# Performance work log

Hardware: AMD Instinct MI355X
Metric: run time of the kernel (lower is better)

Reference implementation:

```python
import jax, jax.numpy as jnp
import numpy as np

HIDDEN = 1024
FRAME = 171
B = 128
T = 256


def _uniform(key, shape, fan):
    bound = 1.0 / np.sqrt(fan)
    return jax.random.uniform(key, shape, jnp.float32, -bound, bound)


def setup_inputs() -> dict:
    key = jax.random.key(0)
    ks = jax.random.split(key, 16)
    H, C = HIDDEN, FRAME
    inp = {
        "seq": jax.random.normal(ks[0], (B, T, C), jnp.float32),
        # LSTMCell 1 (input C -> H); torch layout: weight_ih [4H, in], weight_hh [4H, H]
        "w_ih1": _uniform(ks[1], (4 * H, C), H),
        "w_hh1": _uniform(ks[2], (4 * H, H), H),
        "b_ih1": _uniform(ks[3], (4 * H,), H),
        "b_hh1": _uniform(ks[4], (4 * H,), H),
        # LSTMCell 2 (H -> H)
        "w_ih2": _uniform(ks[5], (4 * H, H), H),
        "w_hh2": _uniform(ks[6], (4 * H, H), H),
        "b_ih2": _uniform(ks[7], (4 * H,), H),
        "b_hh2": _uniform(ks[8], (4 * H,), H),
        # LSTMCell 3 (H -> H)
        "w_ih3": _uniform(ks[9], (4 * H, H), H),
        "w_hh3": _uniform(ks[10], (4 * H, H), H),
        "b_ih3": _uniform(ks[11], (4 * H,), H),
        "b_hh3": _uniform(ks[12], (4 * H,), H),
        # Linear decoder H -> C
        "dec_w": _uniform(ks[13], (C, H), H),
        "dec_b": _uniform(ks[14], (C,), H),
        "gt": 5,
        "cond": 5,
    }
    return inp


def _lstm_cell(x, h, c, w_ih, w_hh, b_ih, b_hh):
    # torch.nn.LSTMCell: gates ordered (i, f, g, o)
    z = x @ w_ih.T + h @ w_hh.T + (b_ih + b_hh)  # [B, 4H]
    i, f, g, o = jnp.split(z, 4, axis=-1)
    c_new = jax.nn.sigmoid(f) * c + jax.nn.sigmoid(i) * jnp.tanh(g)
    h_new = jax.nn.sigmoid(o) * jnp.tanh(c_new)
    return h_new, c_new


def reference(seq, w_ih1, w_hh1, b_ih1, b_hh1,
              w_ih2, w_hh2, b_ih2, b_hh2,
              w_ih3, w_hh3, b_ih3, b_hh3,
              dec_w, dec_b, gt, cond):
    b, t, c = seq.shape
    h = seq.dtype
    # auto-conditioning pattern: gt ground-truth frames then cond self-fed frames
    pattern = (jnp.arange(t) % (gt + cond)) < gt  # [T] bool
    H = w_hh1.shape[1]
    zeros_h = jnp.zeros((b, H), h)
    init = (zeros_h, zeros_h, zeros_h, zeros_h, zeros_h, zeros_h,
            jnp.zeros((b, c), h))

    def step(carry, xs):
        h1, c1, h2, c2, h3, c3, xo = carry
        x_t, p_t = xs
        inp = jnp.where(p_t, x_t, xo)
        h1, c1 = _lstm_cell(inp, h1, c1, w_ih1, w_hh1, b_ih1, b_hh1)
        h2, c2 = _lstm_cell(h1, h2, c2, w_ih2, w_hh2, b_ih2, b_hh2)
        h3, c3 = _lstm_cell(h2, h3, c3, w_ih3, w_hh3, b_ih3, b_hh3)
        out = h3 @ dec_w.T + dec_b  # [B, C]
        return (h1, c1, h2, c2, h3, c3, out), out

    seq_t = jnp.transpose(seq, (1, 0, 2))  # [T, B, C]
    _, outs = jax.lax.scan(step, init, (seq_t, pattern))
    return jnp.transpose(outs, (1, 0, 2))  # [B, T, C]
```

## Files before the change

kernel.cpp:

```cpp
#include <hip/hip_runtime.h>
#include <math.h>

#define TSTEPS 256
#define CDIM 171
#define XSTR 6400
#define SEQB (TSTEPS*CDIM)

#define ARR_OFF   0
#define GF_OFF    2048
#define REL_OFF   2560
#define XCNT_OFF  3072
#define GREG_OFF  3080
#define ARR2_OFF  4096
#define NFLAGS    8192

typedef short v8s __attribute__((ext_vector_type(8)));
typedef float v4f __attribute__((ext_vector_type(4)));
typedef unsigned int v4u __attribute__((ext_vector_type(4)));

static __device__ __forceinline__ unsigned short f2bf(float f) {
  unsigned int u = __float_as_uint(f);
  u += 0x7fffu + ((u >> 16) & 1u);
  return (unsigned short)(u >> 16);
}
static __device__ __forceinline__ float bf2f(unsigned short h) {
  return __uint_as_float(((unsigned int)h) << 16);
}
static __device__ __forceinline__ float sigf(float x) { return 1.0f / (1.0f + expf(-x)); }

static __device__ __forceinline__ bool probe_bf16(const unsigned int* w) {
  int c = 0;
  #pragma unroll
  for (int i = 0; i < 8; ++i) {
    unsigned e = (w[i] >> 7) & 0xFFu;
    c += (e >= 90u && e <= 145u) ? 1 : 0;
  }
  return c == 8;
}
static __device__ __forceinline__ float getv(const void* p, bool bf, size_t i) {
  return bf ? bf2f(((const unsigned short*)p)[i]) : ((const float*)p)[i];
}

static __device__ __forceinline__ unsigned ld_agent(const unsigned* p) {
  return __hip_atomic_load(p, __ATOMIC_RELAXED, __HIP_MEMORY_SCOPE_AGENT);
}
static __device__ __forceinline__ void st_agent(unsigned* p, unsigned v) {
  __hip_atomic_store(p, v, __ATOMIC_RELAXED, __HIP_MEMORY_SCOPE_AGENT);
}
static __device__ __forceinline__ void st_short_sys(unsigned short* p, unsigned short v) {
  asm volatile("global_store_short %0, %1, off sc0 sc1"
               :: "v"(p), "v"((unsigned)v) : "memory");
}
static __device__ __forceinline__ v4u ld_b128_sys(const unsigned short* p) {
  v4u v;
  asm volatile("global_load_dwordx4 %0, %1, off sc0 sc1\n\ts_waitcnt vmcnt(0)"
               : "=v"(v) : "v"(p) : "memory");
  return v;
}

__global__ __launch_bounds__(256) void init_kernel(
    const void* seq, const void* wih1, const void* whh1,
    const void* bih1, const void* bhh1,
    const void* wih2, const void* whh2, const void* bih2, const void* bhh2,
    const void* wih3, const void* whh3, const void* bih3, const void* bhh3,
    const void* decw,
    unsigned short* __restrict__ X, float* __restrict__ BS,
    unsigned* __restrict__ flags,
    unsigned short* __restrict__ WL1, unsigned short* __restrict__ WL2,
    unsigned short* __restrict__ WL3, unsigned short* __restrict__ WDEC,
    unsigned short* __restrict__ XR, unsigned short* __restrict__ XGT,
    const int* __restrict__ gtp, const int* __restrict__ condp)
{
  const int tid = blockIdx.x * 256 + threadIdx.x;
  const int NT = 2048 * 256;
  const bool bfm = probe_bf16((const unsigned int*)seq);
  int gt = gtp[0];
  const bool p0 = 0 < gt;

  for (int i = tid; i < 128 * XSTR; i += NT) {
    int b = i / XSTR, c = i - b * XSTR;
    unsigned short v = 0;
    if (c < CDIM && p0) v = f2bf(getv(seq, bfm, (size_t)b * SEQB + c));
    X[i] = v;
  }
  for (int i = tid; i < 8 * 128 * XSTR; i += NT) {
    int r = i % (128 * XSTR);
    int b = r / XSTR, c = r - b * XSTR;
    unsigned short v = 0;
    if (c < CDIM && p0) v = f2bf(getv(seq, bfm, (size_t)b * SEQB + c));
    XR[i] = v;
  }
  const void* bis[3] = {bih1, bih2, bih3};
  const void* bhs[3] = {bhh1, bhh2, bhh3};
  for (int i = tid; i < 3 * 4096; i += NT) {
    int l = i >> 12, n = i & 4095;
    BS[i] = getv(bis[l], bfm, n) + getv(bhs[l], bfm, n);
  }
  for (int i = tid; i < NFLAGS; i += NT) flags[i] = 0u;
  for (int i = tid; i < 4096 * 1280; i += NT) {
    int r = i / 1280, c = i - r * 1280;
    float v;
    if (c < CDIM)      v = getv(wih1, bfm, (size_t)r * CDIM + c);
    else if (c < 256)  v = 0.f;
    else               v = getv(whh1, bfm, (size_t)r * 1024 + (c - 256));
    WL1[i] = f2bf(v);
  }
  for (int i = tid; i < 4096 * 2048; i += NT) {
    int r = i >> 11, c = i & 2047;
    size_t o = (size_t)r * 1024 + (c & 1023);
    WL2[i] = f2bf((c < 1024) ? getv(wih2, bfm, o) : getv(whh2, bfm, o));
    WL3[i] = f2bf((c < 1024) ? getv(wih3, bfm, o) : getv(whh3, bfm, o));
  }
  for (int i = tid; i < 176 * 1024; i += NT) {
    int r = i >> 10, c = i & 1023;
    WDEC[i] = (r < CDIM) ? f2bf(getv(decw, bfm, (size_t)r * 1024 + c)) : (unsigned short)0;
  }
  if (XGT) {
    for (int i = tid; i < TSTEPS * 128 * 256; i += NT) {
      int t = i >> 15, b = (i >> 8) & 127, c = i & 255;
      unsigned short v = 0;
      if (c < CDIM) v = f2bf(getv(seq, bfm, (size_t)b * SEQB + (size_t)t * CDIM + c));
      XGT[i] = v;
    }
  }
}

static __device__ __forceinline__ void gbar_nf(
    unsigned* fl, unsigned xcd, unsigned rank, unsigned NX, unsigned amask,
    unsigned G, int wave, int lane, unsigned& budget)
{
  __syncthreads();
  if (threadIdx.x == 0) st_agent(fl + ARR_OFF + xcd * 256 + rank, G);
  if (wave == 0) {
    if (rank == 0) {
      const unsigned* ab = fl + ARR_OFF + xcd * 256;
      for (;;) {
        unsigned ok = 1u;
        #pragma unroll
        for (int k = 0; k < 4; ++k) {
          unsigned r = (unsigned)lane + 64u * k;
          if (r < NX) ok &= (ld_agent(ab + r) >= G) ? 1u : 0u;
        }
        if (__all((int)ok)) break;
        if (budget == 0) break;
        --budget; __builtin_amdgcn_s_sleep(1);
      }
      st_agent(fl + GF_OFF + xcd * 64, G);
      for (;;) {
        unsigned ok = 1u;
        if (lane < 8 && ((amask >> lane) & 1u))
          ok = (ld_agent(fl + GF_OFF + (unsigned)lane * 64) >= G) ? 1u : 0u;
        if (__all((int)ok)) break;
        if (budget == 0) break;
        --budget; __builtin_amdgcn_s_sleep(1);
      }
      st_agent(fl + REL_OFF + xcd * 64, G);
    } else {
      unsigned* rp = fl + REL_OFF + xcd * 64;
      for (;;) {
        unsigned v = ld_agent(rp);
        if (__all((int)(v >= G))) break;
        if (budget == 0) break;
        --budget; __builtin_amdgcn_s_sleep(1);
      }
    }
  }
  __syncthreads();
}

static __device__ __forceinline__ void xcopy(
    unsigned short* __restrict__ dst, const unsigned short* __restrict__ src,
    int hoff, int nchunks, int rowshift, unsigned rank, unsigned NX, int tid)
{
  const int mask = (1 << rowshift) - 1;
  for (unsigned c = rank * 256u + (unsigned)tid; c < (unsigned)nchunks;
       c += NX * 256u) {
    int row = (int)(c >> rowshift);
    size_t off = (size_t)row * XSTR + hoff + ((size_t)(c & mask) << 3);
    v4u v = ld_b128_sys(src + off);
    *(v4u*)(dst + off) = v;
  }
}

static __device__ __forceinline__ void xbar(
    unsigned* fl, unsigned xcd, unsigned rank, unsigned NX,
    unsigned G, int wave, int lane, unsigned& budget)
{
  __syncthreads();
  if (threadIdx.x == 0) st_agent(fl + ARR2_OFF + xcd * 256 + rank, G);
  if (wave == 0) {
    const unsigned* ab = fl + ARR2_OFF + xcd * 256;
    for (;;) {
      unsigned ok = 1u;
      #pragma unroll
      for (int k = 0; k < 4; ++k) {
        unsigned r = (unsigned)lane + 64u * k;
        if (r < NX) ok &= (ld_agent(ab + r) >= G) ? 1u : 0u;
      }
      if (__all((int)ok)) break;
      if (budget == 0) break;
      --budget; __builtin_amdgcn_s_sleep(1);
    }
    asm volatile("buffer_inv" ::: "memory");
  }
  __syncthreads();
}

template<int NCH>
static __device__ __forceinline__ void mfma_phase(
    const v8s* wf, const unsigned short* __restrict__ Xb,
    int a0, int bnd, int a1, int kbase, v4f* acc)
{
  #pragma unroll
  for (int i = 0; i < 8; ++i) acc[i] = (v4f){0.f, 0.f, 0.f, 0.f};
  #pragma unroll
  for (int c = 0; c < NCH; ++c) {
    const int acol = kbase + 32 * c;
    const int xcol = (acol < bnd) ? (a0 + acol) : (a1 + acol - bnd);
    const unsigned short* ap = Xb + xcol;
    #pragma unroll
    for (int m = 0; m < 8; ++m) {
      v8s a = *(const v8s*)(ap + (size_t)(16 * m) * XSTR);
      acc[m] = __builtin_amdgcn_mfma_f32_16x16x32_bf16(a, wf[c], acc[m], 0, 0, 0);
    }
  }
}

static __device__ __forceinline__ void lstm_epilogue(
    v4f* acc, float* lred, int wave, int lane,
    const float* bs4, float* cst2,
    unsigned short* __restrict__ X, int hoff, int g)
{
  const int l15 = lane & 15, quad = lane >> 4;
  float* myp = lred + wave * 2048;
  #pragma unroll
  for (int m = 0; m < 8; ++m)
    #pragma unroll
    for (int j = 0; j < 4; ++j)
      myp[m * 256 + l15 * 16 + ((4 * quad + j) ^ ((l15 >> 1) & 3))] = acc[m][j];
  __syncthreads();
  const int ri = lane >> 2, hc = lane & 3;
  #pragma unroll
  for (int e = 0; e < 2; ++e) {
    const int m = 2 * wave + e;
    float z[4];
    #pragma unroll
    for (int k = 0; k < 4; ++k) z[k] = bs4[k];
    #pragma unroll
    for (int w2 = 0; w2 < 4; ++w2) {
      const float* pp = lred + w2 * 2048 + m * 256;
      #pragma unroll
      for (int k = 0; k < 4; ++k) {
        const int col = hc + 4 * k;
        z[k] += pp[col * 16 + (ri ^ ((col >> 1) & 3))];
      }
    }
    float cn = sigf(z[1]) * cst2[e] + sigf(z[0]) * tanhf(z[2]);
    float h  = sigf(z[3]) * tanhf(cn);
    cst2[e] = cn;
    const int row = 32 * wave + 16 * e + ri;
    st_short_sys(X + (size_t)row * XSTR + hoff + 4 * g + hc, f2bf(h));
  }
}

__global__ __launch_bounds__(256, 1) void persist(
    const unsigned short* __restrict__ WL1, const unsigned short* __restrict__ WL2,
    const unsigned short* __restrict__ WL3, const unsigned short* __restrict__ WDEC,
    const float* __restrict__ BS, unsigned short* __restrict__ X,
    unsigned* __restrict__ flags, unsigned short* __restrict__ XR,
    const void* __restrict__ seq, const void* __restrict__ decb,
    void* __restrict__ outp, const unsigned short* __restrict__ XGT,
    const int* __restrict__ gtp, const int* __restrict__ condp)
{
  const int g = blockIdx.x;
  const int tid = threadIdx.x, wave = tid >> 6, lane = tid & 63;
  const int l15 = lane & 15, quad = lane >> 4;
  const bool bf = probe_bf16((const unsigned int*)seq);
  int gt = gtp[0]; int per = gt + condp[0]; if (per < 1) per = 1;
  unsigned budget = 20000000u;

  __shared__ unsigned s_rank;
  unsigned xcd;
  asm volatile("s_getreg_b32 %0, hwreg(HW_REG_XCC_ID)" : "=s"(xcd));
  xcd &= 7u;
  if (tid == 0) {
    s_rank = __hip_atomic_fetch_add(flags + XCNT_OFF + xcd, 1u,
                                    __ATOMIC_RELAXED, __HIP_MEMORY_SCOPE_AGENT);
    __hip_atomic_fetch_add(flags + GREG_OFF, 1u,
                           __ATOMIC_RELEASE, __HIP_MEMORY_SCOPE_AGENT);
  }
  __syncthreads();
  const unsigned rank = s_rank;
  if (wave == 0 && lane == 0) {
    while (__hip_atomic_load(flags + GREG_OFF, __ATOMIC_ACQUIRE,
                             __HIP_MEMORY_SCOPE_AGENT) < 256u) {
      if (budget == 0) break;
      --budget; __builtin_amdgcn_s_sleep(4);
    }
  }
  __syncthreads();
  const unsigned NX = ld_agent(flags + XCNT_OFF + xcd);
  unsigned amask = 0;
  #pragma unroll
  for (int k = 0; k < 8; ++k)
    amask |= (ld_agent(flags + XCNT_OFF + k) > 0u ? 1u : 0u) << k;

  unsigned short* XRb = XR + (size_t)xcd * (128 * XSTR);

  const int br = 1024 * (l15 >> 2) + 4 * g + (l15 & 3);
  v8s w1f[10], w2f[16], w3f[16], wdf[8];
  {
    const unsigned short* p = WL1 + (size_t)br * 1280 + 320 * wave + 8 * quad;
    #pragma unroll
    for (int c = 0; c < 10; ++c) w1f[c] = *(const v8s*)(p + 32 * c);
  }
  {
    const unsigned short* p = WL2 + (size_t)br * 2048 + 512 * wave + 8 * quad;
    #pragma unroll
    for (int c = 0; c < 16; ++c) w2f[c] = *(const v8s*)(p + 32 * c);
  }
  {
    const unsigned short* p = WL3 + (size_t)br * 2048 + 512 * wave + 8 * quad;
    #pragma unroll
    for (int c = 0; c < 16; ++c) w3f[c] = *(const v8s*)(p + 32 * c);
  }
  const int dm = g / 11, dn = g - dm * 11;
  if (g < 88) {
    const unsigned short* p = WDEC + (size_t)(16 * dn + l15) * 1024 + 256 * wave + 8 * quad;
    #pragma unroll
    for (int c = 0; c < 8; ++c) wdf[c] = *(const v8s*)(p + 32 * c);
  } else {
    #pragma unroll
    for (int c = 0; c < 8; ++c) wdf[c] = (v8s){0, 0, 0, 0, 0, 0, 0, 0};
  }
  float bsr[3][4];
  #pragma unroll
  for (int l = 0; l < 3; ++l)
    #pragma unroll
    for (int gm = 0; gm < 4; ++gm)
      bsr[l][gm] = BS[4096 * l + 1024 * gm + 4 * g + (lane & 3)];
  float dbv = 0.f;
  if (g < 88) { int col = 16 * dn + l15; if (col < CDIM) dbv = getv(decb, bf, col); }

  float cst1[2] = {0.f, 0.f}, cst2v[2] = {0.f, 0.f}, cst3[2] = {0.f, 0.f};
  __shared__ float lred[8192];
  const unsigned short* Xb = XRb + (size_t)l15 * XSTR + 8 * quad;
  unsigned bgen = 0;
  v4f acc[8];

  for (int t = 0; t < TSTEPS; ++t) {
    const int p_ = t & 1, q_ = p_ ^ 1;
    const bool pt = (t % per) < gt;
    if (t > 0 && !pt) {
      gbar_nf(flags, xcd, rank, NX, amask, ++bgen, wave, lane, budget);
      xcopy(XRb, X, 0, 4096, 5, rank, NX, tid);
      xbar(flags, xcd, rank, NX, bgen, wave, lane, budget);
    }

    if (pt && wave == 0) {
      #pragma unroll
      for (int i = 0; i < 8; ++i) acc[i] = (v4f){0.f, 0.f, 0.f, 0.f};
      if (XGT) {
        const unsigned short* xb = XGT + ((size_t)t * 128 + l15) * 256 + 8 * quad;
        #pragma unroll
        for (int c = 0; c < 8; ++c) {
          #pragma unroll
          for (int m = 0; m < 8; ++m) {
            v8s a = *(const v8s*)(xb + 32 * c + (size_t)(16 * m) * 256);
            acc[m] = __builtin_amdgcn_mfma_f32_16x16x32_bf16(a, w1f[c], acc[m], 0, 0, 0);
          }
        }
      } else {
        #pragma unroll
        for (int c = 0; c < 8; ++c) {
          const int col0 = 32 * c + 8 * quad;
          #pragma unroll
          for (int m = 0; m < 8; ++m) {
            const size_t so = (size_t)(l15 + 16 * m) * SEQB + (size_t)t * CDIM;
            v8s a;
            #pragma unroll
            for (int j = 0; j < 8; ++j) {
              const int cc = col0 + j;
              unsigned short hv = 0;
              if (cc < CDIM)
                hv = bf ? ((const unsigned short*)seq)[so + cc]
                        : f2bf(((const float*)seq)[so + cc]);
              a[j] = (short)hv;
            }
            acc[m] = __builtin_amdgcn_mfma_f32_16x16x32_bf16(a, w1f[c], acc[m], 0, 0, 0);
          }
        }
      }
      #pragma unroll
      for (int c = 8; c < 10; ++c) {
        const unsigned short* ap = Xb + (256 + 1024 * q_) + (32 * c - 256);
        #pragma unroll
        for (int m = 0; m < 8; ++m) {
          v8s a = *(const v8s*)(ap + (size_t)(16 * m) * XSTR);
          acc[m] = __builtin_amdgcn_mfma_f32_16x16x32_bf16(a, w1f[c], acc[m], 0, 0, 0);
        }
      }
    } else {
      mfma_phase<10>(w1f, Xb, 0, 256, 256 + 1024 * q_, 320 * wave, acc);
    }
    lstm_epilogue(acc, lred, wave, lane, bsr[0], cst1, X, 256 + 1024 * p_, g);

    gbar_nf(flags, xcd, rank, NX, amask, ++bgen, wave, lane, budget);
    xcopy(XRb, X, 256 + 1024 * p_, 16384, 7, rank, NX, tid);
    xbar(flags, xcd, rank, NX, bgen, wave, lane, budget);
    mfma_phase<16>(w2f, Xb, 256 + 1024 * p_, 1024, 2304 + 1024 * q_, 512 * wave, acc);
    lstm_epilogue(acc, lred, wave, lane, bsr[1], cst2v, X, 2304 + 1024 * p_, g);

    gbar_nf(flags, xcd, rank, NX, amask, ++bgen, wave, lane, budget);
    xcopy(XRb, X, 2304 + 1024 * p_, 16384, 7, rank, NX, tid);
    xbar(flags, xcd, rank, NX, bgen, wave, lane, budget);
    mfma_phase<16>(w3f, Xb, 2304 + 1024 * p_, 1024, 4352 + 1024 * q_, 512 * wave, acc);
    lstm_epilogue(acc, lred, wave, lane, bsr[2], cst3, X, 4352 + 1024 * p_, g);

    gbar_nf(flags, xcd, rank, NX, amask, ++bgen, wave, lane, budget);
    xcopy(XRb, X, 4352 + 1024 * p_, 16384, 7, rank, NX, tid);
    xbar(flags, xcd, rank, NX, bgen, wave, lane, budget);
    if (g < 88) {
      v4f da = (v4f){0.f, 0.f, 0.f, 0.f};
      const unsigned short* ap = XRb + (size_t)(16 * dm + l15) * XSTR
                               + (4352 + 1024 * p_) + 256 * wave + 8 * quad;
      #pragma unroll
      for (int c = 0; c < 8; ++c) {
        v8s a = *(const v8s*)(ap + 32 * c);
        da = __builtin_amdgcn_mfma_f32_16x16x32_bf16(a, wdf[c], da, 0, 0, 0);
      }
      float* myp = lred + wave * 2048;
      #pragma unroll
      for (int j = 0; j < 4; ++j)
        myp[l15 * 16 + ((4 * quad + j) ^ ((l15 >> 1) & 3))] = da[j];
      __syncthreads();
      if (wave == 0) {
        const int col = 16 * dn + l15;
        const bool pnext = ((t + 1) % per) < gt;
        #pragma unroll
        for (int e = 0; e < 4; ++e) {
          const int r = 4 * e + quad;
          float v = dbv;
          #pragma unroll
          for (int w2 = 0; w2 < 4; ++w2)
            v += lred[w2 * 2048 + l15 * 16 + (r ^ ((l15 >> 1) & 3))];
          if (col < CDIM) {
            const int brow = 16 * dm + r;
            const size_t oidx = (size_t)brow * SEQB + (size_t)t * CDIM + col;
            if (bf) ((unsigned short*)outp)[oidx] = f2bf(v);
            else    ((float*)outp)[oidx] = v;
            if (t < TSTEPS - 1 && !pnext)
              st_short_sys(X + (size_t)brow * XSTR + col, f2bf(v));
          }
        }
      }
      __syncthreads();
    }
  }
}

extern "C" void kernel_launch(void* const* d_in, const int* in_sizes, int n_in,
                              void* d_out, int out_size, void* d_ws, size_t ws_size,
                              hipStream_t stream) {
  const void* seq  = d_in[0];
  const void* wih1 = d_in[1];  const void* whh1 = d_in[2];
  const void* bih1 = d_in[3];  const void* bhh1 = d_in[4];
  const void* wih2 = d_in[5];  const void* whh2 = d_in[6];
  const void* bih2 = d_in[7];  const void* bhh2 = d_in[8];
  const void* wih3 = d_in[9];  const void* whh3 = d_in[10];
  const void* bih3 = d_in[11]; const void* bhh3 = d_in[12];
  const void* decw = d_in[13]; const void* decb = d_in[14];
  const int* gtp   = (const int*)d_in[15];
  const int* condp = (const int*)d_in[16];

  char* ws = (char*)d_ws;
  unsigned short* X    = (unsigned short*)(ws + 0);
  float*          BS   = (float*)(ws + 1638400);
  unsigned*       FLAGS= (unsigned*)(ws + 1687552);
  unsigned short* XR   = (unsigned short*)(ws + 1720320);
  unsigned short* WL1  = (unsigned short*)(ws + 14827520);
  unsigned short* WL2  = (unsigned short*)(ws + 25313280);
  unsigned short* WL3  = (unsigned short*)(ws + 42090496);
  unsigned short* WDEC = (unsigned short*)(ws + 58867712);
  unsigned short* XGT  = (ws_size >= (size_t)59228160 + (size_t)16777216)
                       ? (unsigned short*)(ws + 59228160) : (unsigned short*)0;

  init_kernel<<<2048, 256, 0, stream>>>(seq, wih1, whh1, bih1, bhh1,
                                        wih2, whh2, bih2, bhh2,
                                        wih3, whh3, bih3, bhh3, decw,
                                        X, BS, FLAGS, WL1, WL2, WL3, WDEC,
                                        XR, XGT, gtp, condp);

  persist<<<256, 256, 0, stream>>>(WL1, WL2, WL3, WDEC, BS, X, FLAGS, XR,
                                   seq, decb, d_out, XGT, gtp, condp);
}
```

Measured before the change: 16.30 ms.

## Compute decoder redundantly per XCD to drop feedback grid barrier

```diff
diff --git a/kernel.cpp b/kernel.cpp
--- a/kernel.cpp
+++ b/kernel.cpp
@@ -16,7 +16,6 @@
 
 typedef short v8s __attribute__((ext_vector_type(8)));
 typedef float v4f __attribute__((ext_vector_type(4)));
-typedef unsigned int v4u __attribute__((ext_vector_type(4)));
 
 static __device__ __forceinline__ unsigned short f2bf(float f) {
   unsigned int u = __float_as_uint(f);
@@ -47,15 +46,8 @@
 static __device__ __forceinline__ void st_agent(unsigned* p, unsigned v) {
   __hip_atomic_store(p, v, __ATOMIC_RELAXED, __HIP_MEMORY_SCOPE_AGENT);
 }
-static __device__ __forceinline__ void st_short_sys(unsigned short* p, unsigned short v) {
-  asm volatile("global_store_short %0, %1, off sc0 sc1"
-               :: "v"(p), "v"((unsigned)v) : "memory");
-}
-static __device__ __forceinline__ v4u ld_b128_sys(const unsigned short* p) {
-  v4u v;
-  asm volatile("global_load_dwordx4 %0, %1, off sc0 sc1\n\ts_waitcnt vmcnt(0)"
-               : "=v"(v) : "v"(p) : "memory");
-  return v;
+static __device__ __forceinline__ void st_agent_us(unsigned short* p, unsigned short v) {
+  __hip_atomic_store(p, v, __ATOMIC_RELAXED, __HIP_MEMORY_SCOPE_AGENT);
 }
 
 __global__ __launch_bounds__(256) void init_kernel(
@@ -170,15 +162,28 @@
 
 static __device__ __forceinline__ void xcopy(
     unsigned short* __restrict__ dst, const unsigned short* __restrict__ src,
-    int hoff, int nchunks, int rowshift, unsigned rank, unsigned NX, int tid)
-{
-  const int mask = (1 << rowshift) - 1;
-  for (unsigned c = rank * 256u + (unsigned)tid; c < (unsigned)nchunks;
-       c += NX * 256u) {
-    int row = (int)(c >> rowshift);
-    size_t off = (size_t)row * XSTR + hoff + ((size_t)(c & mask) << 3);
-    v4u v = ld_b128_sys(src + off);
-    *(v4u*)(dst + off) = v;
+    int hoff, unsigned rank, unsigned NX, int tid)
+{
+  if (NX == 32u) {
+    const unsigned d0 = rank * 256u + (unsigned)tid;
+    unsigned vv[8];
+    #pragma unroll
+    for (int k = 0; k < 8; ++k) {
+      unsigned d = d0 + 8192u * k;
+      size_t off = (size_t)(d >> 9) * XSTR + hoff + ((size_t)(d & 511u) << 1);
+      vv[k] = ld_agent((const unsigned*)(src + off));
+    }
+    #pragma unroll
+    for (int k = 0; k < 8; ++k) {
+      unsigned d = d0 + 8192u * k;
+      size_t off = (size_t)(d >> 9) * XSTR + hoff + ((size_t)(d & 511u) << 1);
+      *(unsigned*)(dst + off) = vv[k];
+    }
+  } else {
+    for (unsigned d = rank * 256u + (unsigned)tid; d < 65536u; d += NX * 256u) {
+      size_t off = (size_t)(d >> 9) * XSTR + hoff + ((size_t)(d & 511u) << 1);
+      *(unsigned*)(dst + off) = ld_agent((const unsigned*)(src + off));
+    }
   }
 }
 
@@ -259,8 +264,55 @@
     float h  = sigf(z[3]) * tanhf(cn);
     cst2[e] = cn;
     const int row = 32 * wave + 16 * e + ri;
-    st_short_sys(X + (size_t)row * XSTR + hoff + 4 * g + hc, f2bf(h));
-  }
+    st_agent_us(X + (size_t)row * XSTR + hoff + 4 * g + hc, f2bf(h));
+  }
+}
+
+static __device__ __forceinline__ void dec_tile(
+    int dm2, int dn2, const unsigned short* __restrict__ WDEC,
+    const unsigned short* __restrict__ XRb, int p_, float* lred,
+    int wave, int lane, int l15, int quad,
+    const void* __restrict__ decb, bool bf, bool wout, bool wx,
+    void* __restrict__ outp, int t)
+{
+  v4f da = (v4f){0.f, 0.f, 0.f, 0.f};
+  const unsigned short* wp = WDEC + (size_t)(16 * dn2 + l15) * 1024 + 256 * wave + 8 * quad;
+  const unsigned short* ap = XRb + (size_t)(16 * dm2 + l15) * XSTR
+                           + (4352 + 1024 * p_) + 256 * wave + 8 * quad;
+  #pragma unroll
+  for (int c = 0; c < 8; ++c) {
+    v8s a = *(const v8s*)(ap + 32 * c);
+    v8s w = *(const v8s*)(wp + 32 * c);
+    da = __builtin_amdgcn_mfma_f32_16x16x32_bf16(a, w, da, 0, 0, 0);
+  }
+  float* myp = lred + wave * 2048;
+  #pragma unroll
+  for (int j = 0; j < 4; ++j)
+    myp[l15 * 16 + ((4 * quad + j) ^ ((l15 >> 1) & 3))] = da[j];
+  __syncthreads();
+  if (wave == 0) {
+    const int col = 16 * dn2 + l15;
+    float dbv2 = (col < CDIM) ? getv(decb, bf, col) : 0.f;
+    #pragma unroll
+    for (int e = 0; e < 4; ++e) {
+      const int r = 4 * e + quad;
+      float v = dbv2;
+      #pragma unroll
+      for (int w2 = 0; w2 < 4; ++w2)
+        v += lred[w2 * 2048 + l15 * 16 + (r ^ ((l15 >> 1) & 3))];
+      if (col < CDIM) {
+        const int brow = 16 * dm2 + r;
+        if (wout) {
+          const size_t oidx = (size_t)brow * SEQB + (size_t)t * CDIM + col;
+          if (bf) ((unsigned short*)outp)[oidx] = f2bf(v);
+          else    ((float*)outp)[oidx] = v;
+        }
+        if (wx) *(unsigned short*)((unsigned short*)XRb
+                  + (size_t)brow * XSTR + col) = f2bf(v);
+      }
+    }
+  }
+  __syncthreads();
 }
 
 __global__ __launch_bounds__(256, 1) void persist(
@@ -304,11 +356,13 @@
   #pragma unroll
   for (int k = 0; k < 8; ++k)
     amask |= (ld_agent(flags + XCNT_OFF + k) > 0u ? 1u : 0u) << k;
+  const unsigned owner = (unsigned)__builtin_ctz(amask | 0x100u);
+  const bool isown = (xcd == owner);
 
   unsigned short* XRb = XR + (size_t)xcd * (128 * XSTR);
 
   const int br = 1024 * (l15 >> 2) + 4 * g + (l15 & 3);
-  v8s w1f[10], w2f[16], w3f[16], wdf[8];
+  v8s w1f[10], w2f[16], w3f[16];
   {
     const unsigned short* p = WL1 + (size_t)br * 1280 + 320 * wave + 8 * quad;
     #pragma unroll
@@ -325,22 +379,12 @@
     for (int c = 0; c < 16; ++c) w3f[c] = *(const v8s*)(p + 32 * c);
   }
   const int dm = g / 11, dn = g - dm * 11;
-  if (g < 88) {
-    const unsigned short* p = WDEC + (size_t)(16 * dn + l15) * 1024 + 256 * wave + 8 * quad;
-    #pragma unroll
-    for (int c = 0; c < 8; ++c) wdf[c] = *(const v8s*)(p + 32 * c);
-  } else {
-    #pragma unroll
-    for (int c = 0; c < 8; ++c) wdf[c] = (v8s){0, 0, 0, 0, 0, 0, 0, 0};
-  }
   float bsr[3][4];
   #pragma unroll
   for (int l = 0; l < 3; ++l)
     #pragma unroll
     for (int gm = 0; gm < 4; ++gm)
       bsr[l][gm] = BS[4096 * l + 1024 * gm + 4 * g + (lane & 3)];
-  float dbv = 0.f;
-  if (g < 88) { int col = 16 * dn + l15; if (col < CDIM) dbv = getv(decb, bf, col); }
 
   float cst1[2] = {0.f, 0.f}, cst2v[2] = {0.f, 0.f}, cst3[2] = {0.f, 0.f};
   __shared__ float lred[8192];
@@ -351,11 +395,6 @@
   for (int t = 0; t < TSTEPS; ++t) {
     const int p_ = t & 1, q_ = p_ ^ 1;
     const bool pt = (t % per) < gt;
-    if (t > 0 && !pt) {
-      gbar_nf(flags, xcd, rank, NX, amask, ++bgen, wave, lane, budget);
-      xcopy(XRb, X, 0, 4096, 5, rank, NX, tid);
-      xbar(flags, xcd, rank, NX, bgen, wave, lane, budget);
-    }
 
     if (pt && wave == 0) {
       #pragma unroll
@@ -406,55 +445,34 @@
     lstm_epilogue(acc, lred, wave, lane, bsr[0], cst1, X, 256 + 1024 * p_, g);
 
     gbar_nf(flags, xcd, rank, NX, amask, ++bgen, wave, lane, budget);
-    xcopy(XRb, X, 256 + 1024 * p_, 16384, 7, rank, NX, tid);
+    xcopy(XRb, X, 256 + 1024 * p_, rank, NX, tid);
     xbar(flags, xcd, rank, NX, bgen, wave, lane, budget);
     mfma_phase<16>(w2f, Xb, 256 + 1024 * p_, 1024, 2304 + 1024 * q_, 512 * wave, acc);
     lstm_epilogue(acc, lred, wave, lane, bsr[1], cst2v, X, 2304 + 1024 * p_, g);
 
     gbar_nf(flags, xcd, rank, NX, amask, ++bgen, wave, lane, budget);
-    xcopy(XRb, X, 2304 + 1024 * p_, 16384, 7, rank, NX, tid);
+    xcopy(XRb, X, 2304 + 1024 * p_, rank, NX, tid);
     xbar(flags, xcd, rank, NX, bgen, wave, lane, budget);
     mfma_phase<16>(w3f, Xb, 2304 + 1024 * p_, 1024, 4352 + 1024 * q_, 512 * wave, acc);
     lstm_epilogue(acc, lred, wave, lane, bsr[2], cst3, X, 4352 + 1024 * p_, g);
 
     gbar_nf(flags, xcd, rank, NX, amask, ++bgen, wave, lane, budget);
-    xcopy(XRb, X, 4352 + 1024 * p_, 16384, 7, rank, NX, tid);
+    xcopy(XRb, X, 4352 + 1024 * p_, rank, NX, tid);
     xbar(flags, xcd, rank, NX, bgen, wave, lane, budget);
-    if (g < 88) {
-      v4f da = (v4f){0.f, 0.f, 0.f, 0.f};
-      const unsigned short* ap = XRb + (size_t)(16 * dm + l15) * XSTR
-                               + (4352 + 1024 * p_) + 256 * wave + 8 * quad;
-      #pragma unroll
-      for (int c = 0; c < 8; ++c) {
-        v8s a = *(const v8s*)(ap + 32 * c);
-        da = __builtin_amdgcn_mfma_f32_16x16x32_bf16(a, wdf[c], da, 0, 0, 0);
-      }
-      float* myp = lred + wave * 2048;
-      #pragma unroll
-      for (int j = 0; j < 4; ++j)
-        myp[l15 * 16 + ((4 * quad + j) ^ ((l15 >> 1) & 3))] = da[j];
-      __syncthreads();
-      if (wave == 0) {
-        const int col = 16 * dn + l15;
-        const bool pnext = ((t + 1) % per) < gt;
-        #pragma unroll
-        for (int e = 0; e < 4; ++e) {
-          const int r = 4 * e + quad;
-          float v = dbv;
-          #pragma unroll
-          for (int w2 = 0; w2 < 4; ++w2)
-            v += lred[w2 * 2048 + l15 * 16 + (r ^ ((l15 >> 1) & 3))];
-          if (col < CDIM) {
-            const int brow = 16 * dm + r;
-            const size_t oidx = (size_t)brow * SEQB + (size_t)t * CDIM + col;
-            if (bf) ((unsigned short*)outp)[oidx] = f2bf(v);
-            else    ((float*)outp)[oidx] = v;
-            if (t < TSTEPS - 1 && !pnext)
-              st_short_sys(X + (size_t)brow * XSTR + col, f2bf(v));
-          }
-        }
-      }
-      __syncthreads();
+
+    const bool pnext = ((t + 1) % per) < gt;
+    const bool needx = (t < TSTEPS - 1) && !pnext;
+    if (needx) {
+      for (unsigned tt = rank; tt < 88u; tt += NX) {
+        int dm2 = (int)(tt / 11u), dn2 = (int)(tt - (unsigned)dm2 * 11u);
+        dec_tile(dm2, dn2, WDEC, XRb, p_, lred, wave, lane, l15, quad,
+                 decb, bf, isown, true, outp, t);
+      }
+      ++bgen;
+      xbar(flags, xcd, rank, NX, bgen, wave, lane, budget);
+    } else if (g < 88) {
+      dec_tile(dm, dn, WDEC, XRb, p_, lred, wave, lane, l15, quad,
+               decb, bf, true, false, outp, t);
     }
   }
 }
```

Result: no change. 16.06 ms (-1.5%).
